# Performance work log

Measured on AMD Instinct MI355X. Metric: run time of the kernel, lower is better.

## Reference

```python
import jax, jax.numpy as jnp
import numpy as np


def setup_inputs() -> dict:
    key = jax.random.key(0)
    k1, k2 = jax.random.split(key)
    B, H, L = 8, 768, 4096
    x = jax.random.normal(k1, (B, H, L), dtype=jnp.float32)
    k = jax.random.normal(k2, (H, L), dtype=jnp.float32)
    return {"x": x, "k": k, "n": L}


def reference(x, k, n):
    # FFT-based long convolution: fft(x) * fft(k), inverse fft, real part,
    # truncated to the input sequence length. Inputs are real, so rfft/irfft
    # compute the identical result to complex fft + .real, at half the work.
    L = x.shape[-1]
    xf = jnp.fft.rfft(x, n=n)                 # [B, H, n//2+1] complex
    kf = jnp.fft.rfft(k, n=n)                 # [H, n//2+1]   complex
    y = jnp.fft.irfft(xf * kf, n=n)[..., :L]  # [B, H, L]
    return y.astype(x.dtype)
```

## Files before the change

kernel.cpp:

```cpp
#include <hip/hip_runtime.h>
#include <math.h>


#define NT 512
#define KF_LD 2049
#define C_SQRT1_2 0.70710678118654752f
#define INV_4096 2.44140625e-4f

#define SW(a) ((a) ^ (((a) >> 5) & 31) ^ (((a) >> 2) & 24))
__device__ __forceinline__ int WP(int a) {
  const int s = SW(a);
  return 2 * s - (s & 63);
}

__device__ __forceinline__ void sincos_rev(float f, float& sn, float& cs) {
  float s_, c_;
  asm("v_sin_f32 %0, %1" : "=v"(s_) : "v"(f));
  asm("v_cos_f32 %0, %1" : "=v"(c_) : "v"(f));
  sn = s_; cs = c_;
}

template <int SIGN>
__device__ __forceinline__ void bf8(const float ar[8], const float ai[8],
                                    float br[8], float bi[8]) {
  float s0r = ar[0] + ar[4], s0i = ai[0] + ai[4];
  float s1r = ar[0] - ar[4], s1i = ai[0] - ai[4];
  float s2r = ar[2] + ar[6], s2i = ai[2] + ai[6];
  float s3r = ar[2] - ar[6], s3i = ai[2] - ai[6];
  float E0r = s0r + s2r, E0i = s0i + s2i;
  float E2r = s0r - s2r, E2i = s0i - s2i;
  float E1r, E1i, E3r, E3i;
  if (SIGN < 0) { E1r = s1r + s3i; E1i = s1i - s3r; E3r = s1r - s3i; E3i = s1i + s3r; }
  else          { E1r = s1r - s3i; E1i = s1i + s3r; E3r = s1r + s3i; E3i = s1i - s3r; }
  float u0r = ar[1] + ar[5], u0i = ai[1] + ai[5];
  float u1r = ar[1] - ar[5], u1i = ai[1] - ai[5];
  float u2r = ar[3] + ar[7], u2i = ai[3] + ai[7];
  float u3r = ar[3] - ar[7], u3i = ai[3] - ai[7];
  float O0r = u0r + u2r, O0i = u0i + u2i;
  float O2r = u0r - u2r, O2i = u0i - u2i;
  float O1r, O1i, O3r, O3i;
  if (SIGN < 0) { O1r = u1r + u3i; O1i = u1i - u3r; O3r = u1r - u3i; O3i = u1i + u3r; }
  else          { O1r = u1r - u3i; O1i = u1i + u3r; O3r = u1r + u3i; O3i = u1i - u3r; }
  float t1r, t1i, t2r, t2i, t3r, t3i;
  if (SIGN < 0) {
    t1r = C_SQRT1_2 * (O1r + O1i); t1i = C_SQRT1_2 * (O1i - O1r);
    t2r = O2i;  t2i = -O2r;
    t3r = C_SQRT1_2 * (O3i - O3r); t3i = -C_SQRT1_2 * (O3r + O3i);
  } else {
    t1r = C_SQRT1_2 * (O1r - O1i); t1i = C_SQRT1_2 * (O1i + O1r);
    t2r = -O2i; t2i = O2r;
    t3r = -C_SQRT1_2 * (O3r + O3i); t3i = C_SQRT1_2 * (O3r - O3i);
  }
  br[0] = E0r + O0r; bi[0] = E0i + O0i;
  br[4] = E0r - O0r; bi[4] = E0i - O0i;
  br[1] = E1r + t1r; bi[1] = E1i + t1i;
  br[5] = E1r - t1r; bi[5] = E1i - t1i;
  br[2] = E2r + t2r; bi[2] = E2i + t2i;
  br[6] = E2r - t2r; bi[6] = E2i - t2i;
  br[3] = E3r + t3r; bi[3] = E3i + t3i;
  br[7] = E3r - t3r; bi[7] = E3i - t3i;
}

template <int SIGN, int S>
__device__ __forceinline__ void tw_write(float* Z, int ob,
                                         const float br[8], const float bi[8],
                                         float f1) {
  { const int i0 = WP(ob); Z[i0] = br[0]; Z[i0 + 64] = bi[0]; }
  float sn, cs;
  sincos_rev(f1, sn, cs);
  const float w1r = cs, w1i = (SIGN > 0) ? sn : -sn;
  float cwr = w1r, cwi = w1i;
#pragma unroll
  for (int m = 1; m < 8; ++m) {
    const int idx = WP(ob + S * m);
    Z[idx] = br[m] * cwr - bi[m] * cwi;
    Z[idx + 64] = br[m] * cwi + bi[m] * cwr;
    if (m < 7) {
      const float nr = cwr * w1r - cwi * w1i;
      const float ni = cwr * w1i + cwi * w1r;
      cwr = nr; cwi = ni;
    }
  }
}

template <int SIGN, int S>
__device__ __forceinline__ void stage_r8_ip(float* Z, const int rd[8]) {
  const int t = (int)threadIdx.x;
  const int q = t & (S - 1);
  const int p = t / S;
  float ar[8], ai[8];
#pragma unroll
  for (int j = 0; j < 8; ++j) {
    ar[j] = Z[rd[j]];
    ai[j] = Z[rd[j] + 64];
  }
  __syncthreads();
  float br[8], bi[8];
  bf8<SIGN>(ar, ai, br, bi);
  tw_write<SIGN, S>(Z, q + 8 * S * p, br, bi, (float)(S * p) * INV_4096);
  __syncthreads();
}

__device__ __forceinline__ void stage1_conv(const float* __restrict__ x0,
                                            const float* __restrict__ x1,
                                            float* Z) {
  const int t = (int)threadIdx.x;
  float ar[8], ai[8];
#pragma unroll
  for (int j = 0; j < 8; ++j) {
    ar[j] = x0[t + 512 * j];
    ai[j] = x1[t + 512 * j];
  }
  float br[8], bi[8];
  bf8<-1>(ar, ai, br, bi);
  tw_write<-1, 1>(Z, 8 * t, br, bi, (float)t * INV_4096);
}

__device__ __forceinline__ void stage4_kf(float* Z,
                                          const float2* __restrict__ kfrow,
                                          const int rd[8]) {
  const int t = (int)threadIdx.x;
  float ar[8], ai[8];
#pragma unroll
  for (int j = 0; j < 8; ++j) {
    ar[j] = Z[rd[j]];
    ai[j] = Z[rd[j] + 64];
  }
  float br[8], bi[8];
  bf8<-1>(ar, ai, br, bi);
#pragma unroll
  for (int m = 0; m < 8; ++m) {
    const int k = t + 512 * m;
    float2 kv;
    if (m <= 3) {
      kv = kfrow[k];
    } else {
      kv = kfrow[4096 - k];
      kv.y = -kv.y;
    }
    const int i = rd[m];
    Z[i] = br[m] * kv.x - bi[m] * kv.y;
    Z[i + 64] = br[m] * kv.y + bi[m] * kv.x;
  }
}

__device__ __forceinline__ void stage4_store(const float* Z,
                                             float* __restrict__ y0,
                                             float* __restrict__ y1,
                                             const int rd[8]) {
  const int t = (int)threadIdx.x;
  float ar[8], ai[8];
#pragma unroll
  for (int j = 0; j < 8; ++j) {
    ar[j] = Z[rd[j]];
    ai[j] = Z[rd[j] + 64];
  }
  float br[8], bi[8];
  bf8<1>(ar, ai, br, bi);
#pragma unroll
  for (int m = 0; m < 8; ++m) {
    const int k = t + 512 * m;
    y0[k] = br[m];
    y1[k] = bi[m];
  }
}

__device__ __forceinline__ void stage1_k(const float* __restrict__ kin,
                                         float* Z) {
  const int t = (int)threadIdx.x;
  float ar[8], ai[8];
#pragma unroll
  for (int j = 0; j < 8; ++j) {
    ar[j] = kin[t + 512 * j];
    ai[j] = 0.0f;
  }
  float br[8], bi[8];
  bf8<-1>(ar, ai, br, bi);
  tw_write<-1, 1>(Z, 8 * t, br, bi, (float)t * INV_4096);
}

__device__ __forceinline__ void stage4_kstore(const float* Z,
                                              float2* __restrict__ kfrow,
                                              const int rd[8]) {
  const int t = (int)threadIdx.x;
  float ar[8], ai[8];
#pragma unroll
  for (int j = 0; j < 8; ++j) {
    ar[j] = Z[rd[j]];
    ai[j] = Z[rd[j] + 64];
  }
  float br[8], bi[8];
  bf8<-1>(ar, ai, br, bi);
  const float sc = 1.0f / 4096.0f;
#pragma unroll
  for (int m = 0; m < 4; ++m) {
    const int k = t + 512 * m;
    kfrow[k] = make_float2(br[m] * sc, bi[m] * sc);
  }
  if (t == 0) kfrow[2048] = make_float2(br[4] * sc, bi[4] * sc);
}

__global__ __launch_bounds__(NT) void kfft_kernel(const float* __restrict__ kin,
                                                  float2* __restrict__ kf) {
  __shared__ float Z_[8192];
  const int t = (int)threadIdx.x;
  const int h = (int)blockIdx.x;
  int rd[8];
#pragma unroll
  for (int j = 0; j < 8; ++j) rd[j] = WP(t + 512 * j);
  stage1_k(kin + (size_t)h * 4096, Z_);
  __syncthreads();
  stage_r8_ip<-1, 8>(Z_, rd);
  stage_r8_ip<-1, 64>(Z_, rd);
  stage4_kstore(Z_, kf + (size_t)h * KF_LD, rd);
}

__global__ __launch_bounds__(NT) void conv_kernel(const float* __restrict__ x,
                                                  const float2* __restrict__ kf,
                                                  float* __restrict__ y, int H) {
  __shared__ float Z_[8192];
  const int bi = (int)blockIdx.x;
  const int h = bi % H;
  const int j = bi / H;
  const size_t r0 = (size_t)(2 * j) * H + h;
  const size_t r1 = r0 + H;
  const float* src0 = x + r0 * 4096;
  const float* src1 = x + r1 * 4096;
  float* dst0 = y + r0 * 4096;
  float* dst1 = y + r1 * 4096;
  const float2* kfrow = kf + (size_t)h * KF_LD;
  const int t = (int)threadIdx.x;
  int rd[8];
#pragma unroll
  for (int jj = 0; jj < 8; ++jj) rd[jj] = WP(t + 512 * jj);
  stage1_conv(src0, src1, Z_);
  __syncthreads();
  stage_r8_ip<-1, 8>(Z_, rd);
  stage_r8_ip<-1, 64>(Z_, rd);
  stage4_kf(Z_, kfrow, rd);
  __syncthreads();
  stage_r8_ip<1, 1>(Z_, rd);
  stage_r8_ip<1, 8>(Z_, rd);
  stage_r8_ip<1, 64>(Z_, rd);
  stage4_store(Z_, dst0, dst1, rd);
}

extern "C" void kernel_launch(void* const* d_in, const int* in_sizes, int n_in,
                              void* d_out, int out_size, void* d_ws, size_t ws_size,
                              hipStream_t stream) {
  const float* x = (const float*)d_in[0];
  const float* kin = (const float*)d_in[1];
  float* y = (float*)d_out;
  const int H = in_sizes[1] / 4096;
  const int BH = in_sizes[0] / 4096;
  float2* kf = (float2*)d_ws;
  hipLaunchKernelGGL(kfft_kernel, dim3(H), dim3(NT), 0, stream, kin, kf);
  hipLaunchKernelGGL(conv_kernel, dim3(BH / 2), dim3(NT), 0, stream, x, kf, y, H);
}
```

Before: 64.65 us.

## Fuse forward last stage with inverse first stage and loop multiple pairs per block

The last forward radix-8 stage, the pointwise multiply by the kernel spectrum, and the first inverse radix-8 stage now run in one register pass. This removes one shared-memory round trip and one barrier per row pair. Each block also processes NPB=3 row pairs in a loop, which cuts the block count and amortises setup such as index computation. The cost is fewer blocks in flight (1024 instead of 3072), which can leave the device with less parallelism and less latency hiding.

```diff
diff --git a/kernel.cpp b/kernel.cpp
--- a/kernel.cpp
+++ b/kernel.cpp
@@ -3,6 +3,7 @@
 
 
 #define NT 512
+#define NPB 3
 #define KF_LD 2049
 #define C_SQRT1_2 0.70710678118654752f
 #define INV_4096 2.44140625e-4f
@@ -116,9 +117,9 @@
   tw_write<-1, 1>(Z, 8 * t, br, bi, (float)t * INV_4096);
 }
 
-__device__ __forceinline__ void stage4_kf(float* Z,
-                                          const float2* __restrict__ kfrow,
-                                          const int rd[8]) {
+__device__ __forceinline__ void stage_mid_ip(float* Z,
+                                             const float2* __restrict__ kfrow,
+                                             const int rd[8]) {
   const int t = (int)threadIdx.x;
   float ar[8], ai[8];
 #pragma unroll
@@ -126,6 +127,7 @@
     ar[j] = Z[rd[j]];
     ai[j] = Z[rd[j] + 64];
   }
+  __syncthreads();
   float br[8], bi[8];
   bf8<-1>(ar, ai, br, bi);
 #pragma unroll
@@ -138,10 +140,12 @@
       kv = kfrow[4096 - k];
       kv.y = -kv.y;
     }
-    const int i = rd[m];
-    Z[i] = br[m] * kv.x - bi[m] * kv.y;
-    Z[i + 64] = br[m] * kv.y + bi[m] * kv.x;
-  }
+    ar[m] = br[m] * kv.x - bi[m] * kv.y;
+    ai[m] = br[m] * kv.y + bi[m] * kv.x;
+  }
+  bf8<1>(ar, ai, br, bi);
+  tw_write<1, 1>(Z, 8 * t, br, bi, (float)t * INV_4096);
+  __syncthreads();
 }
 
 __device__ __forceinline__ void stage4_store(const float* Z,
@@ -165,41 +169,6 @@
   }
 }
 
-__device__ __forceinline__ void stage1_k(const float* __restrict__ kin,
-                                         float* Z) {
-  const int t = (int)threadIdx.x;
-  float ar[8], ai[8];
-#pragma unroll
-  for (int j = 0; j < 8; ++j) {
-    ar[j] = kin[t + 512 * j];
-    ai[j] = 0.0f;
-  }
-  float br[8], bi[8];
-  bf8<-1>(ar, ai, br, bi);
-  tw_write<-1, 1>(Z, 8 * t, br, bi, (float)t * INV_4096);
-}
-
-__device__ __forceinline__ void stage4_kstore(const float* Z,
-                                              float2* __restrict__ kfrow,
-                                              const int rd[8]) {
-  const int t = (int)threadIdx.x;
-  float ar[8], ai[8];
-#pragma unroll
-  for (int j = 0; j < 8; ++j) {
-    ar[j] = Z[rd[j]];
-    ai[j] = Z[rd[j] + 64];
-  }
-  float br[8], bi[8];
-  bf8<-1>(ar, ai, br, bi);
-  const float sc = 1.0f / 4096.0f;
-#pragma unroll
-  for (int m = 0; m < 4; ++m) {
-    const int k = t + 512 * m;
-    kfrow[k] = make_float2(br[m] * sc, bi[m] * sc);
-  }
-  if (t == 0) kfrow[2048] = make_float2(br[4] * sc, bi[4] * sc);
-}
-
 __global__ __launch_bounds__(NT) void kfft_kernel(const float* __restrict__ kin,
                                                   float2* __restrict__ kf) {
   __shared__ float Z_[8192];
@@ -208,41 +177,67 @@
   int rd[8];
 #pragma unroll
   for (int j = 0; j < 8; ++j) rd[j] = WP(t + 512 * j);
-  stage1_k(kin + (size_t)h * 4096, Z_);
+  {
+    const float* src = kin + (size_t)h * 4096;
+    float ar[8], ai[8];
+#pragma unroll
+    for (int j = 0; j < 8; ++j) { ar[j] = src[t + 512 * j]; ai[j] = 0.0f; }
+    float br[8], bi[8];
+    bf8<-1>(ar, ai, br, bi);
+    tw_write<-1, 1>(Z_, 8 * t, br, bi, (float)t * INV_4096);
+  }
   __syncthreads();
   stage_r8_ip<-1, 8>(Z_, rd);
   stage_r8_ip<-1, 64>(Z_, rd);
-  stage4_kstore(Z_, kf + (size_t)h * KF_LD, rd);
+  {
+    float ar[8], ai[8];
+#pragma unroll
+    for (int j = 0; j < 8; ++j) { ar[j] = Z_[rd[j]]; ai[j] = Z_[rd[j] + 64]; }
+    float br[8], bi[8];
+    bf8<-1>(ar, ai, br, bi);
+    const float sc = 1.0f / 4096.0f;
+    float2* kfrow = kf + (size_t)h * KF_LD;
+#pragma unroll
+    for (int m = 0; m < 4; ++m) {
+      const int k = t + 512 * m;
+      kfrow[k] = make_float2(br[m] * sc, bi[m] * sc);
+    }
+    if (t == 0) kfrow[2048] = make_float2(br[4] * sc, bi[4] * sc);
+  }
 }
 
 __global__ __launch_bounds__(NT) void conv_kernel(const float* __restrict__ x,
                                                   const float2* __restrict__ kf,
-                                                  float* __restrict__ y, int H) {
+                                                  float* __restrict__ y, int H,
+                                                  int pairs) {
   __shared__ float Z_[8192];
-  const int bi = (int)blockIdx.x;
-  const int h = bi % H;
-  const int j = bi / H;
-  const size_t r0 = (size_t)(2 * j) * H + h;
-  const size_t r1 = r0 + H;
-  const float* src0 = x + r0 * 4096;
-  const float* src1 = x + r1 * 4096;
-  float* dst0 = y + r0 * 4096;
-  float* dst1 = y + r1 * 4096;
-  const float2* kfrow = kf + (size_t)h * KF_LD;
   const int t = (int)threadIdx.x;
   int rd[8];
 #pragma unroll
   for (int jj = 0; jj < 8; ++jj) rd[jj] = WP(t + 512 * jj);
-  stage1_conv(src0, src1, Z_);
-  __syncthreads();
-  stage_r8_ip<-1, 8>(Z_, rd);
-  stage_r8_ip<-1, 64>(Z_, rd);
-  stage4_kf(Z_, kfrow, rd);
-  __syncthreads();
-  stage_r8_ip<1, 1>(Z_, rd);
-  stage_r8_ip<1, 8>(Z_, rd);
-  stage_r8_ip<1, 64>(Z_, rd);
-  stage4_store(Z_, dst0, dst1, rd);
+  const int p0 = (int)blockIdx.x * NPB;
+#pragma unroll 1
+  for (int ii = 0; ii < NPB; ++ii) {
+    const int p = p0 + ii;
+    if (p >= pairs) break;
+    const int h = p % H;
+    const int b2 = p / H;
+    const size_t r0 = ((size_t)(2 * b2) * H + (size_t)h) * 4096;
+    const float* src0 = x + r0;
+    const float* src1 = src0 + (size_t)H * 4096;
+    float* dst0 = y + r0;
+    float* dst1 = dst0 + (size_t)H * 4096;
+    const float2* kfrow = kf + (size_t)h * KF_LD;
+    stage1_conv(src0, src1, Z_);
+    __syncthreads();
+    stage_r8_ip<-1, 8>(Z_, rd);
+    stage_r8_ip<-1, 64>(Z_, rd);
+    stage_mid_ip(Z_, kfrow, rd);
+    stage_r8_ip<1, 8>(Z_, rd);
+    stage_r8_ip<1, 64>(Z_, rd);
+    stage4_store(Z_, dst0, dst1, rd);
+    __syncthreads();
+  }
 }
 
 extern "C" void kernel_launch(void* const* d_in, const int* in_sizes, int n_in,
@@ -253,7 +248,10 @@
   float* y = (float*)d_out;
   const int H = in_sizes[1] / 4096;
   const int BH = in_sizes[0] / 4096;
+  const int pairs = BH / 2;
+  const int blocks = (pairs + NPB - 1) / NPB;
   float2* kf = (float2*)d_ws;
   hipLaunchKernelGGL(kfft_kernel, dim3(H), dim3(NT), 0, stream, kin, kf);
-  hipLaunchKernelGGL(conv_kernel, dim3(BH / 2), dim3(NT), 0, stream, x, kf, y, H);
-}
+  hipLaunchKernelGGL(conv_kernel, dim3(blocks), dim3(NT), 0, stream, x, kf, y,
+                     H, pairs);
+}
```

After: 59.98 us. -7.2%, faster.
